# Performance work log

Hardware: AMD Instinct MI355X
Metric: run time of the kernel (lower is better)

Reference implementation:

```python
import jax, jax.numpy as jnp
import numpy as np

NHLOG2PI = -0.5 * np.log(2.0 * np.pi)


def _log_bessel_i(nu, x):
    # log I_nu(x) via the uniform asymptotic expansion (A&S 9.7.7), accurate for large nu.
    # Replaces the original mpmath besseli loop with a device-friendly closed form.
    z = x / nu
    sq = jnp.sqrt(1.0 + z * z)
    eta = sq + jnp.log(z) - jnp.log1p(sq)
    t = 1.0 / sq
    u1 = (3.0 * t - 5.0 * t ** 3) / 24.0  # first correction term
    return nu * eta - 0.5 * jnp.log(2.0 * jnp.pi * nu) - 0.25 * jnp.log1p(z * z) + jnp.log1p(u1 / nu)


def _log_vmf_partition(d, kappa):
    # log C_d(kappa) = d*(-0.5 log 2pi) + s*log(kappa) - log I_s(kappa), s = d/2 - 1
    s = 0.5 * d - 1.0
    return d * NHLOG2PI + s * jnp.log(kappa) - _log_bessel_i(s, kappa)


def reference(id_samples, kappa_weight, prototypes, targets, project_dim):
    eps_n = 1e-12  # torch F.normalize eps
    eps_c = 1e-8   # torch cosine_similarity eps
    # --- sequential normalized EMA scatter-update of prototypes (faithful to per-sample loop) ---
    norm_samples = id_samples / jnp.maximum(
        jnp.linalg.norm(id_samples, axis=-1, keepdims=True), eps_n)

    def step(protos, inp):
        s_n, t = inp
        new = 0.05 * s_n + 0.95 * protos[t]
        new = new / jnp.maximum(jnp.linalg.norm(new), eps_n)
        return protos.at[t].set(new), None

    protos, _ = jax.lax.scan(step, prototypes, (norm_samples, targets))
    protos = jax.lax.stop_gradient(protos)  # original uses .data.detach()

    # --- cosine similarity [N, C] without materializing the repeated tensors ---
    x_n = id_samples / jnp.maximum(jnp.linalg.norm(id_samples, axis=-1, keepdims=True), eps_c)
    p_n = protos / jnp.maximum(jnp.linalg.norm(protos, axis=-1, keepdims=True), eps_c)
    cos = x_n @ p_n.T  # [N, C]

    kap = jax.nn.relu(kappa_weight)  # [C]
    logits = cos * kap[None, :]
    weight_before_exp = jnp.exp(_log_vmf_partition(float(project_dim), kap))[None, :]  # [1, C]

    # --- weighted vMF NLL ---
    num = weight_before_exp * jnp.exp(logits)
    pred = num / num.sum(-1, keepdims=True)
    p_t = jnp.take_along_axis(pred, targets[:, None], axis=1)[:, 0]
    return -jnp.mean(jnp.log(p_t + 1e-6))


def setup_inputs() -> dict:
    key = jax.random.key(0)
    k1, k2, k3 = jax.random.split(key, 3)
    N, C, D = 16384, 2048, 32
    return {
        "id_samples": jax.random.normal(k1, (N, D), dtype=jnp.float32),
        "kappa_weight": jax.random.uniform(k2, (C,), dtype=jnp.float32),
        "prototypes": jnp.zeros((C, D), dtype=jnp.float32),
        "targets": jax.random.randint(k3, (N,), 0, C),
        "project_dim": D,
    }
```

## Files before the change

kernel.cpp:

```cpp
#include <hip/hip_runtime.h>
#include <hip/hip_bf16.h>
#include <math.h>

#define D 32
#define CAP 64
#define PRE 24
#define SBT 512

typedef __attribute__((ext_vector_type(8))) short short8v;
typedef __attribute__((ext_vector_type(4))) float float4v;

static __device__ __forceinline__ unsigned short f2bf(float f) {
    union { __hip_bfloat16 h; unsigned short u; } cv;
    cv.h = __float2bfloat16(f);
    return cv.u;
}

__global__ void k_bucket(const int* __restrict__ tgt, int* __restrict__ cnt,
                         int* __restrict__ list2d, int N) {
    int i = blockIdx.x * blockDim.x + threadIdx.x;
    if (i < N) {
        int t = tgt[i];
        int pos = atomicAdd(&cnt[t], 1);
        if (pos < CAP) list2d[t * CAP + pos] = i;
    }
}

__global__ void k_proto(const float* __restrict__ x, const int* __restrict__ tgt,
                        const int* __restrict__ list2d, const int* __restrict__ cnt,
                        const float* __restrict__ p_in, const float* __restrict__ kw,
                        unsigned short* __restrict__ qb, float* __restrict__ w,
                        int N, int C, float dval) {
    int wave = (blockIdx.x * blockDim.x + threadIdx.x) >> 6;
    int lane = threadIdx.x & 63;
    if (wave >= C) return;
    int c = wave, e = lane & 31;
    float p = p_in[(size_t)c * D + e];
    int count = cnt[c];

    if (count <= PRE) {
        int idx = (lane < count) ? list2d[c * CAP + lane] : 0x7fffffff;
        int rank = 0;
        for (int j = 0; j < count; ++j) {
            int v = __shfl(idx, j);
            rank += (v < idx) ? 1 : 0;
        }
        int sorted = 0;
        for (int j = 0; j < count; ++j) {
            int v = __shfl(idx, j); int r = __shfl(rank, j);
            if (r == lane) sorted = v;
        }
        float vals[PRE];
#pragma unroll
        for (int it = 0; it < PRE; ++it)
            if (it < count) {
                int si = __shfl(sorted, it);
                vals[it] = x[(size_t)si * D + e];
            }
#pragma unroll
        for (int it = 0; it < PRE; ++it)
            if (it < count) {
                float v = vals[it];
                float ss = v * v;
                ss += __shfl_xor(ss, 16); ss += __shfl_xor(ss, 8); ss += __shfl_xor(ss, 4);
                ss += __shfl_xor(ss, 2);  ss += __shfl_xor(ss, 1);
                vals[it] = v / fmaxf(sqrtf(ss), 1e-12f);
            }
#pragma unroll
        for (int it = 0; it < PRE; ++it)
            if (it < count) {
                p = fmaf(0.05f, vals[it], 0.95f * p);
                float pp = p * p;
                pp += __shfl_xor(pp, 16); pp += __shfl_xor(pp, 8); pp += __shfl_xor(pp, 4);
                pp += __shfl_xor(pp, 2);  pp += __shfl_xor(pp, 1);
                p = p / fmaxf(sqrtf(pp), 1e-12f);
            }
    } else if (count <= CAP) {
        int idx = (lane < count) ? list2d[c * CAP + lane] : 0x7fffffff;
        for (int it = 0; it < count; ++it) {
            int mn = idx;
            mn = min(mn, __shfl_xor(mn, 32)); mn = min(mn, __shfl_xor(mn, 16));
            mn = min(mn, __shfl_xor(mn, 8));  mn = min(mn, __shfl_xor(mn, 4));
            mn = min(mn, __shfl_xor(mn, 2));  mn = min(mn, __shfl_xor(mn, 1));
            float v = x[(size_t)mn * D + e];
            float ss = v * v;
            ss += __shfl_xor(ss, 16); ss += __shfl_xor(ss, 8); ss += __shfl_xor(ss, 4);
            ss += __shfl_xor(ss, 2);  ss += __shfl_xor(ss, 1);
            float s = v / fmaxf(sqrtf(ss), 1e-12f);
            p = fmaf(0.05f, s, 0.95f * p);
            float pp = p * p;
            pp += __shfl_xor(pp, 16); pp += __shfl_xor(pp, 8); pp += __shfl_xor(pp, 4);
            pp += __shfl_xor(pp, 2);  pp += __shfl_xor(pp, 1);
            p = p / fmaxf(sqrtf(pp), 1e-12f);
            if (idx == mn) idx = 0x7fffffff;
        }
    } else {
        for (int ii = 0; ii < N; ii += 64) {
            unsigned long long m = __ballot(tgt[ii + lane] == c);
            while (m) {
                int j = __ffsll(m) - 1;
                m &= (m - 1);
                float v = x[(size_t)(ii + j) * D + e];
                float ss = v * v;
                ss += __shfl_xor(ss, 16); ss += __shfl_xor(ss, 8); ss += __shfl_xor(ss, 4);
                ss += __shfl_xor(ss, 2);  ss += __shfl_xor(ss, 1);
                float s = v / fmaxf(sqrtf(ss), 1e-12f);
                p = fmaf(0.05f, s, 0.95f * p);
                float pp = p * p;
                pp += __shfl_xor(pp, 16); pp += __shfl_xor(pp, 8); pp += __shfl_xor(pp, 4);
                pp += __shfl_xor(pp, 2);  pp += __shfl_xor(pp, 1);
                p = p / fmaxf(sqrtf(pp), 1e-12f);
            }
        }
    }

    float pp = p * p;
    pp += __shfl_xor(pp, 16); pp += __shfl_xor(pp, 8); pp += __shfl_xor(pp, 4);
    pp += __shfl_xor(pp, 2);  pp += __shfl_xor(pp, 1);
    float pn = p / fmaxf(sqrtf(pp), 1e-8f);
    float kap = fmaxf(kw[c], 0.0f);
    if (lane < D) qb[(size_t)c * D + e] = f2bf(kap * pn);
    if (lane == 0) {
        float nu = 0.5f * dval - 1.0f;
        float z  = kap / nu, z2 = z * z;
        float sq = sqrtf(1.0f + z2);
        float t  = 1.0f / sq;
        float u1 = (3.0f * t - 5.0f * t * t * t) * (1.0f / 24.0f);
        float lw = dval * (-0.918938533204672742f)
                 + nu * (logf(nu) + log1pf(sq) - sq)
                 + 0.5f * logf(6.2831853071795864f * nu)
                 + 0.25f * log1pf(z2)
                 - log1pf(u1 / nu);
        w[c] = __expf(lw);
    }
}

__global__ void __launch_bounds__(SBT)
k_score(const float* __restrict__ x, const int* __restrict__ tgt,
        const unsigned short* __restrict__ qb, const float* __restrict__ w,
        float* __restrict__ part, int N, int C) {
    __shared__ float Sl[8][32];
    __shared__ float Lt[32];
    int tid = threadIdx.x, b = blockIdx.x;
    int lane = tid & 63, wv = tid >> 6;
    int m = lane & 15, kg = lane >> 4, k0 = kg * 8;
    int s0 = b * 32;

    short8v a0, a1;
    {
        const float4* px = (const float4*)(x + (size_t)(s0 + m) * D + k0);
        float4 u0 = px[0], u1 = px[1];
        float ss = u0.x*u0.x + u0.y*u0.y + u0.z*u0.z + u0.w*u0.w
                 + u1.x*u1.x + u1.y*u1.y + u1.z*u1.z + u1.w*u1.w;
        ss += __shfl_xor(ss, 16); ss += __shfl_xor(ss, 32);
        float inv = 1.0f / fmaxf(sqrtf(ss), 1e-8f);
        a0[0] = (short)f2bf(u0.x*inv); a0[1] = (short)f2bf(u0.y*inv);
        a0[2] = (short)f2bf(u0.z*inv); a0[3] = (short)f2bf(u0.w*inv);
        a0[4] = (short)f2bf(u1.x*inv); a0[5] = (short)f2bf(u1.y*inv);
        a0[6] = (short)f2bf(u1.z*inv); a0[7] = (short)f2bf(u1.w*inv);
    }
    {
        const float4* px = (const float4*)(x + (size_t)(s0 + 16 + m) * D + k0);
        float4 u0 = px[0], u1 = px[1];
        float ss = u0.x*u0.x + u0.y*u0.y + u0.z*u0.z + u0.w*u0.w
                 + u1.x*u1.x + u1.y*u1.y + u1.z*u1.z + u1.w*u1.w;
        ss += __shfl_xor(ss, 16); ss += __shfl_xor(ss, 32);
        float inv = 1.0f / fmaxf(sqrtf(ss), 1e-8f);
        a1[0] = (short)f2bf(u0.x*inv); a1[1] = (short)f2bf(u0.y*inv);
        a1[2] = (short)f2bf(u0.z*inv); a1[3] = (short)f2bf(u0.w*inv);
        a1[4] = (short)f2bf(u1.x*inv); a1[5] = (short)f2bf(u1.y*inv);
        a1[6] = (short)f2bf(u1.z*inv); a1[7] = (short)f2bf(u1.w*inv);
    }

    int tr0[4], tr1[4];
#pragma unroll
    for (int r = 0; r < 4; ++r) {
        tr0[r] = tgt[s0 + kg * 4 + r];
        tr1[r] = tgt[s0 + 16 + kg * 4 + r];
    }

    float4v z = {0.f, 0.f, 0.f, 0.f};
    float4v sa0 = z, sa1 = z;
    int ntiles = C / (16 * 8);
    for (int jt = 0; jt < ntiles; ++jt) {
        int c0 = (wv * ntiles + jt) * 16;
        short8v bfrag = *(const short8v*)(qb + (size_t)(c0 + m) * D + k0);
        float wl = w[c0 + m];
        float4v acc0 = __builtin_amdgcn_mfma_f32_16x16x32_bf16(a0, bfrag, z, 0, 0, 0);
        float4v acc1 = __builtin_amdgcn_mfma_f32_16x16x32_bf16(a1, bfrag, z, 0, 0, 0);
#pragma unroll
        for (int r = 0; r < 4; ++r) {
            if (c0 + m == tr0[r]) Lt[kg * 4 + r] = acc0[r];
            if (c0 + m == tr1[r]) Lt[16 + kg * 4 + r] = acc1[r];
            sa0[r] = fmaf(wl, __expf(acc0[r]), sa0[r]);
            sa1[r] = fmaf(wl, __expf(acc1[r]), sa1[r]);
        }
    }
#pragma unroll
    for (int off = 1; off < 16; off <<= 1) {
#pragma unroll
        for (int r = 0; r < 4; ++r) {
            sa0[r] += __shfl_xor(sa0[r], off);
            sa1[r] += __shfl_xor(sa1[r], off);
        }
    }
    if (m == 0) {
#pragma unroll
        for (int r = 0; r < 4; ++r) {
            Sl[wv][kg * 4 + r]      = sa0[r];
            Sl[wv][16 + kg * 4 + r] = sa1[r];
        }
    }
    __syncthreads();

    if (wv == 0) {
        float val = 0.f;
        if (lane < 32) {
            int s = lane;
            float S = ((Sl[0][s] + Sl[1][s]) + (Sl[2][s] + Sl[3][s]))
                    + ((Sl[4][s] + Sl[5][s]) + (Sl[6][s] + Sl[7][s]));
            int t = tgt[s0 + s];
            val = logf(w[t] * __expf(Lt[s]) / S + 1e-6f);
        }
        val += __shfl_xor(val, 32); val += __shfl_xor(val, 16); val += __shfl_xor(val, 8);
        val += __shfl_xor(val, 4);  val += __shfl_xor(val, 2);  val += __shfl_xor(val, 1);
        if (lane == 0) part[b] = val;
    }
}

__global__ void k_out(const float* __restrict__ part, float* __restrict__ out,
                      int N, int nblk) {
    __shared__ float red[8];
    int tid = threadIdx.x, lane = tid & 63, wv = tid >> 6;
    float v = (tid < nblk) ? part[tid] : 0.f;
    v += __shfl_xor(v, 32); v += __shfl_xor(v, 16); v += __shfl_xor(v, 8);
    v += __shfl_xor(v, 4);  v += __shfl_xor(v, 2);  v += __shfl_xor(v, 1);
    if (lane == 0) red[wv] = v;
    __syncthreads();
    if (tid == 0)
        out[0] = -(((red[0] + red[1]) + (red[2] + red[3]))
                 + ((red[4] + red[5]) + (red[6] + red[7]))) / (float)N;
}

extern "C" void kernel_launch(void* const* d_in, const int* in_sizes, int n_in,
                              void* d_out, int out_size, void* d_ws, size_t ws_size,
                              hipStream_t stream) {
    const float* x    = (const float*)d_in[0];
    const float* kw   = (const float*)d_in[1];
    const float* p_in = (const float*)d_in[2];
    const int*   tgt  = (const int*)d_in[3];
    int C = in_sizes[1];
    int N = in_sizes[3];
    float dval = (float)(in_sizes[2] / C);
    int nblk = N / 32;

    int* cnt = (int*)d_ws;
    size_t zbytes = ((size_t)C * sizeof(int) + 63) & ~(size_t)63;
    unsigned short* qb = (unsigned short*)((char*)d_ws + zbytes);
    float* w    = (float*)(qb + (size_t)C * D);
    float* part = w + C;
    int* list2d = (int*)(part + nblk);
    (void)n_in; (void)out_size; (void)ws_size;

    hipMemsetAsync(cnt, 0, (size_t)C * sizeof(int), stream);
    k_bucket<<<(N + 255) / 256, 256, 0, stream>>>(tgt, cnt, list2d, N);
    k_proto<<<(C * 64 + 255) / 256, 256, 0, stream>>>(x, tgt, list2d, cnt, p_in, kw, qb, w, N, C, dval);
    k_score<<<nblk, SBT, 0, stream>>>(x, tgt, qb, w, part, N, C);
    k_out<<<1, 512, 0, stream>>>(part, (float*)d_out, N, nblk);
}
```

Baseline: 44.14 us.

## Fuse target bucketing into prototype kernel with per-block shared-memory lists

```diff
diff --git a/kernel.cpp b/kernel.cpp
--- a/kernel.cpp
+++ b/kernel.cpp
@@ -5,6 +5,7 @@
 #define D 32
 #define CAP 64
 #define PRE 24
+#define PBW 8
 #define SBT 512
 
 typedef __attribute__((ext_vector_type(8))) short short8v;
@@ -16,30 +17,36 @@
     return cv.u;
 }
 
-__global__ void k_bucket(const int* __restrict__ tgt, int* __restrict__ cnt,
-                         int* __restrict__ list2d, int N) {
-    int i = blockIdx.x * blockDim.x + threadIdx.x;
-    if (i < N) {
+__global__ void __launch_bounds__(64 * PBW)
+k_pb(const float* __restrict__ x, const int* __restrict__ tgt,
+     const float* __restrict__ p_in, const float* __restrict__ kw,
+     unsigned short* __restrict__ qb, float* __restrict__ w,
+     int N, int C, float dval) {
+    __shared__ int lcnt[PBW];
+    __shared__ int llist[PBW][CAP];
+    int tid = threadIdx.x, b = blockIdx.x;
+    int lane = tid & 63, wv = tid >> 6;
+    int c0 = b * PBW;
+
+    if (tid < PBW) lcnt[tid] = 0;
+    __syncthreads();
+    for (int i = tid; i < N; i += 64 * PBW) {
         int t = tgt[i];
-        int pos = atomicAdd(&cnt[t], 1);
-        if (pos < CAP) list2d[t * CAP + pos] = i;
-    }
-}
-
-__global__ void k_proto(const float* __restrict__ x, const int* __restrict__ tgt,
-                        const int* __restrict__ list2d, const int* __restrict__ cnt,
-                        const float* __restrict__ p_in, const float* __restrict__ kw,
-                        unsigned short* __restrict__ qb, float* __restrict__ w,
-                        int N, int C, float dval) {
-    int wave = (blockIdx.x * blockDim.x + threadIdx.x) >> 6;
-    int lane = threadIdx.x & 63;
-    if (wave >= C) return;
-    int c = wave, e = lane & 31;
+        int r = t - c0;
+        if ((unsigned)r < (unsigned)PBW) {
+            int pos = atomicAdd(&lcnt[r], 1);
+            if (pos < CAP) llist[r][pos] = i;
+        }
+    }
+    __syncthreads();
+
+    int c = c0 + wv;
+    int e = lane & 31;
     float p = p_in[(size_t)c * D + e];
-    int count = cnt[c];
+    int count = lcnt[wv];
 
     if (count <= PRE) {
-        int idx = (lane < count) ? list2d[c * CAP + lane] : 0x7fffffff;
+        int idx = (lane < count) ? llist[wv][lane] : 0x7fffffff;
         int rank = 0;
         for (int j = 0; j < count; ++j) {
             int v = __shfl(idx, j);
@@ -76,7 +83,7 @@
                 p = p / fmaxf(sqrtf(pp), 1e-12f);
             }
     } else if (count <= CAP) {
-        int idx = (lane < count) ? list2d[c * CAP + lane] : 0x7fffffff;
+        int idx = (lane < count) ? llist[wv][lane] : 0x7fffffff;
         for (int it = 0; it < count; ++it) {
             int mn = idx;
             mn = min(mn, __shfl_xor(mn, 32)); mn = min(mn, __shfl_xor(mn, 16));
@@ -254,17 +261,12 @@
     float dval = (float)(in_sizes[2] / C);
     int nblk = N / 32;
 
-    int* cnt = (int*)d_ws;
-    size_t zbytes = ((size_t)C * sizeof(int) + 63) & ~(size_t)63;
-    unsigned short* qb = (unsigned short*)((char*)d_ws + zbytes);
+    unsigned short* qb = (unsigned short*)d_ws;
     float* w    = (float*)(qb + (size_t)C * D);
     float* part = w + C;
-    int* list2d = (int*)(part + nblk);
     (void)n_in; (void)out_size; (void)ws_size;
 
-    hipMemsetAsync(cnt, 0, (size_t)C * sizeof(int), stream);
-    k_bucket<<<(N + 255) / 256, 256, 0, stream>>>(tgt, cnt, list2d, N);
-    k_proto<<<(C * 64 + 255) / 256, 256, 0, stream>>>(x, tgt, list2d, cnt, p_in, kw, qb, w, N, C, dval);
+    k_pb<<<C / PBW, 64 * PBW, 0, stream>>>(x, tgt, p_in, kw, qb, w, N, C, dval);
     k_score<<<nblk, SBT, 0, stream>>>(x, tgt, qb, w, part, N, C);
     k_out<<<1, 512, 0, stream>>>(part, (float*)d_out, N, nblk);
 }
```

New measurement: 40.51 us. -8.2%, faster.
